# Performance work log

Measured on AMD Instinct MI355X. Metric: run time of the kernel, lower is better.

Reference implementation:

```python
import jax, jax.numpy as jnp
import numpy as np

EPS = 1e-5

def layer_norm(x, g, b):
    m = jnp.mean(x, axis=-1, keepdims=True)
    v = jnp.mean((x - m) ** 2, axis=-1, keepdims=True)
    return (x - m) * jax.lax.rsqrt(v + EPS) * g + b

def setup_inputs() -> dict:
    key = jax.random.key(0)
    ks = jax.random.split(key, 16)
    B, S, IN, D, K = 32, 4096, 256, 64, 8
    inputs = jax.random.normal(ks[0], (B, S, IN), dtype=jnp.float32)
    mask = jnp.ones((B, S), dtype=jnp.int32)
    slot_emb = jax.random.normal(ks[1], (1, K, D), dtype=jnp.float32)
    Wq = jax.random.normal(ks[2], (D, D), dtype=jnp.float32) / np.sqrt(D)
    Wk = jax.random.normal(ks[3], (IN, D), dtype=jnp.float32) / np.sqrt(IN)
    Wv = jax.random.normal(ks[4], (IN, D), dtype=jnp.float32) / np.sqrt(IN)
    W_ih = jax.random.normal(ks[5], (D, 3 * D), dtype=jnp.float32) / np.sqrt(D)
    W_hh = jax.random.normal(ks[6], (D, 3 * D), dtype=jnp.float32) / np.sqrt(D)
    b_ih = jnp.zeros((3 * D,), dtype=jnp.float32)
    b_hh = jnp.zeros((3 * D,), dtype=jnp.float32)
    ln_in_g = jnp.ones((IN,), dtype=jnp.float32)
    ln_in_b = jnp.zeros((IN,), dtype=jnp.float32)
    ln_s_g = jnp.ones((D,), dtype=jnp.float32)
    ln_s_b = jnp.zeros((D,), dtype=jnp.float32)
    Wval = jax.random.normal(ks[7], (D, 1), dtype=jnp.float32) / np.sqrt(D)
    bval = jnp.zeros((1,), dtype=jnp.float32)
    return dict(inputs=inputs, mask=mask, slot_emb=slot_emb, Wq=Wq, Wk=Wk, Wv=Wv,
                W_ih=W_ih, W_hh=W_hh, b_ih=b_ih, b_hh=b_hh,
                ln_in_g=ln_in_g, ln_in_b=ln_in_b, ln_s_g=ln_s_g, ln_s_b=ln_s_b,
                Wval=Wval, bval=bval)

def gru_cell(x, h, W_ih, W_hh, b_ih, b_hh):
    # PyTorch GRUCell: gates ordered (r, z, n)
    gx = x @ W_ih + b_ih
    gh = h @ W_hh + b_hh
    D = h.shape[-1]
    gx_r, gx_z, gx_n = gx[..., :D], gx[..., D:2 * D], gx[..., 2 * D:]
    gh_r, gh_z, gh_n = gh[..., :D], gh[..., D:2 * D], gh[..., 2 * D:]
    r = jax.nn.sigmoid(gx_r + gh_r)
    z = jax.nn.sigmoid(gx_z + gh_z)
    n = jnp.tanh(gx_n + r * gh_n)
    return (1.0 - z) * n + z * h

def reference(inputs, mask, slot_emb, Wq, Wk, Wv, W_ih, W_hh, b_ih, b_hh,
              ln_in_g, ln_in_b, ln_s_g, ln_s_b, Wval, bval):
    B, S, _ = inputs.shape
    K, D = slot_emb.shape[1], slot_emb.shape[2]
    num_iterations = 3
    slots = jnp.broadcast_to(slot_emb, (B, K, D))
    # inputs are constant across iterations: hoist norm + k/v projections
    inputs_norm = layer_norm(inputs, ln_in_g, ln_in_b)
    k = inputs_norm @ Wk  # [B, S, D]
    v = inputs_norm @ Wv  # [B, S, D]
    neg_big = jnp.finfo(inputs.dtype).min
    mask_bks = (mask[:, None, :] == 0)  # [B, 1, S] -> broadcast to [B, K, S]
    scale = 1.0 / np.sqrt(D)
    attn = None
    for _ in range(num_iterations):
        slots_norm = layer_norm(slots, ln_s_g, ln_s_b)
        q = slots_norm @ Wq  # [B, K, D]
        scores = jnp.einsum('bkd,bsd->bks', q, k) * scale
        scores = jnp.where(mask_bks, neg_big, scores)
        attn = jax.nn.softmax(scores, axis=-1)  # [B, K, S]
        updates = jnp.einsum('bks,bsd->bkd', attn, v)  # [B, K, D]
        slots = gru_cell(updates.reshape(-1, D), slots.reshape(-1, D),
                         W_ih, W_hh, b_ih, b_hh).reshape(B, K, D)
    validity = (slots @ Wval + bval)[..., 0]  # [B, K]
    slot_mask = (validity > 0).astype(jnp.float32)  # eval-mode (deterministic) path
    return slots, attn, slot_mask
```

## Files before the change

kernel.cpp:

```cpp
#include <hip/hip_runtime.h>

typedef unsigned short u16;
typedef unsigned int   u32;
typedef _Float16 f16x8 __attribute__((ext_vector_type(8)));
typedef u32    u32x4 __attribute__((ext_vector_type(4)));
typedef float  f32x4 __attribute__((ext_vector_type(4)));

#define NEG_BIG (-3.4028234663852886e38f)
#define LO_SCALE 2048.0f
#define LO_INV   (1.0f/2048.0f)

__device__ __forceinline__ u32 splitpack(float x){
  _Float16 h = (_Float16)x;
  _Float16 l = (_Float16)((x - (float)h) * LO_SCALE);
  return (u32)__builtin_bit_cast(u16, h) | ((u32)__builtin_bit_cast(u16, l) << 16);
}
__device__ __forceinline__ void split2(float x, _Float16& h, _Float16& l){
  h = (_Float16)x;
  l = (_Float16)((x - (float)h) * LO_SCALE);
}
__device__ __forceinline__ void unpack8(const u32* p, f16x8& h, f16x8& l){
  #pragma unroll
  for (int j = 0; j < 8; j++){
    u32 v = p[j];
    h[j] = __builtin_bit_cast(_Float16, (u16)(v & 0xFFFFu));
    l[j] = __builtin_bit_cast(_Float16, (u16)(v >> 16));
  }
}
__device__ __forceinline__ float wsum(float v){
  #pragma unroll
  for (int m = 32; m >= 1; m >>= 1) v += __shfl_xor(v, m, 64);
  return v;
}
__device__ __forceinline__ float wmax(float v){
  #pragma unroll
  for (int m = 32; m >= 1; m >>= 1) v = fmaxf(v, __shfl_xor(v, m, 64));
  return v;
}

__global__ __launch_bounds__(256, 2)
void k_proj(const float* __restrict__ in, const float* __restrict__ g,
            const float* __restrict__ bb, const float* __restrict__ Wk,
            const float* __restrict__ Wv, u32* __restrict__ kws,
            u32* __restrict__ vws)
{
  __shared__ u32 A[64 * 258];
  const int t = threadIdx.x, w = t >> 6, l = t & 63, q = l >> 4, l15 = l & 15;
  const long base = (long)blockIdx.x * 64;

  f32x4 xv[16];
  const f32x4* in4 = (const f32x4*)in;
  #pragma unroll
  for (int i = 0; i < 16; i++) xv[i] = in4[(base + i*4 + w) * 64 + l];

  const f32x4 gv = ((const f32x4*)g)[l];
  const f32x4 bv = ((const f32x4*)bb)[l];

  #pragma unroll
  for (int i = 0; i < 16; i++){
    f32x4 x = xv[i];
    float s  = x.x + x.y + x.z + x.w;
    float ss = x.x*x.x + x.y*x.y + x.z*x.z + x.w*x.w;
    s = wsum(s); ss = wsum(ss);
    float mean = s * (1.f/256.f);
    float var  = fmaxf(ss * (1.f/256.f) - mean*mean, 0.f);
    float rstd = rsqrtf(var + 1e-5f);
    int row = i*4 + w;
    u32x4 o;
    o[0] = splitpack((x.x - mean) * rstd * gv.x + bv.x);
    o[1] = splitpack((x.y - mean) * rstd * gv.y + bv.y);
    o[2] = splitpack((x.z - mean) * rstd * gv.z + bv.z);
    o[3] = splitpack((x.w - mean) * rstd * gv.w + bv.w);
    *(u32x4*)&A[row*258 + l*4] = o;
  }
  __syncthreads();

  f32x4 a1[4][2] = {};
  f32x4 a2[4][2] = {};

  #pragma unroll
  for (int half = 0; half < 2; half++){
    f16x8 bh[2][4], bl[2][4];
    #pragma unroll
    for (int n2 = 0; n2 < 2; n2++){
      const int n = w*32 + n2*16 + l15;
      const float* src = (n < 64) ? (Wk + n) : (Wv + (n - 64));
      #pragma unroll
      for (int k4 = 0; k4 < 4; k4++){
        #pragma unroll
        for (int j = 0; j < 8; j++){
          float wv = src[((half*4 + k4)*32 + q*8 + j) * 64];
          _Float16 h, lo; split2(wv, h, lo);
          bh[n2][k4][j] = h; bl[n2][k4][j] = lo;
        }
      }
    }
    #pragma unroll
    for (int k4 = 0; k4 < 4; k4++){
      const int kt = half*4 + k4;
      f16x8 ah[4], al[4];
      #pragma unroll
      for (int mt = 0; mt < 4; mt++)
        unpack8(&A[(mt*16 + l15)*258 + kt*32 + q*8], ah[mt], al[mt]);
      #pragma unroll
      for (int mt = 0; mt < 4; mt++)
        #pragma unroll
        for (int n2 = 0; n2 < 2; n2++){
          a1[mt][n2] = __builtin_amdgcn_mfma_f32_16x16x32_f16(ah[mt], bh[n2][k4], a1[mt][n2], 0,0,0);
          a2[mt][n2] = __builtin_amdgcn_mfma_f32_16x16x32_f16(ah[mt], bl[n2][k4], a2[mt][n2], 0,0,0);
          a2[mt][n2] = __builtin_amdgcn_mfma_f32_16x16x32_f16(al[mt], bh[n2][k4], a2[mt][n2], 0,0,0);
        }
    }
  }
  __syncthreads();

  #pragma unroll
  for (int mt = 0; mt < 4; mt++)
    #pragma unroll
    for (int n2 = 0; n2 < 2; n2++)
      #pragma unroll
      for (int r = 0; r < 4; r++){
        int row = mt*16 + q*4 + r;
        int col = w*32 + n2*16 + l15;
        A[row*130 + col] = splitpack(a1[mt][n2][r] + a2[mt][n2][r] * LO_INV);
      }
  __syncthreads();

  const int b  = (int)(base >> 12);
  const int s0 = (int)(base & 4095);
  for (int task = t; task < 1024; task += 256){
    int row = task >> 4, seg = task & 15;
    u32x4 val = *(const u32x4*)&A[row*130 + seg*4];
    *(u32x4*)(kws + ((long)b*4096 + s0 + row)*64 + seg*4) = val;
  }
  for (int task = t; task < 1024; task += 256){
    int d = task >> 4, seg = task & 15;
    u32x4 vv;
    #pragma unroll
    for (int j = 0; j < 4; j++) vv[j] = A[(seg*4 + j)*130 + 64 + d];
    *(u32x4*)(vws + ((long)b*64 + d)*4096 + s0 + seg*4) = vv;
  }
}

__global__ __launch_bounds__(256)
void k_attn_part(const float* __restrict__ qws, const u32* __restrict__ kws,
                 const u32* __restrict__ vws, const int* __restrict__ mask,
                 float* __restrict__ scores, float* __restrict__ part)
{
  __shared__ float pl[8 * 256];
  __shared__ u32   pb[16 * 258];
  __shared__ float ml[8];
  const int c = blockIdx.x, b = blockIdx.y;
  const int t = threadIdx.x, w = t >> 6, l = t & 63, q = l >> 4, l15 = l & 15;

  f16x8 qh[2], ql[2];
  #pragma unroll
  for (int kt = 0; kt < 2; kt++){
    #pragma unroll
    for (int j = 0; j < 8; j++){
      int d = kt*32 + q*8 + j;
      float qv = (l15 < 8) ? qws[b*512 + l15*64 + d] : 0.f;
      _Float16 h, lo; split2(qv, h, lo);
      qh[kt][j] = h; ql[kt][j] = lo;
    }
  }
  f32x4 s1[4] = {}, s2[4] = {};
  #pragma unroll
  for (int kt = 0; kt < 2; kt++)
    #pragma unroll
    for (int mt = 0; mt < 4; mt++){
      const u32* kr = kws + ((long)b*4096 + c*256 + w*64 + mt*16 + l15)*64
                      + kt*32 + q*8;
      f16x8 ah, al; unpack8(kr, ah, al);
      s1[mt] = __builtin_amdgcn_mfma_f32_16x16x32_f16(ah, qh[kt], s1[mt], 0,0,0);
      s2[mt] = __builtin_amdgcn_mfma_f32_16x16x32_f16(ah, ql[kt], s2[mt], 0,0,0);
      s2[mt] = __builtin_amdgcn_mfma_f32_16x16x32_f16(al, qh[kt], s2[mt], 0,0,0);
    }
  #pragma unroll
  for (int mt = 0; mt < 4; mt++)
    #pragma unroll
    for (int r = 0; r < 4; r++)
      if (l15 < 8)
        pl[l15*256 + w*64 + mt*16 + q*4 + r] = s1[mt][r] + s2[mt][r] * LO_INV;
  __syncthreads();

  const int s = c*256 + t;
  const int mk = mask[b*4096 + s];
  float sc[8];
  #pragma unroll
  for (int k8 = 0; k8 < 8; k8++){
    float v0 = pl[k8*256 + t] * 0.125f;
    sc[k8] = mk ? v0 : NEG_BIG;
    scores[((long)(b*8 + k8))*4096 + s] = sc[k8];
    pl[k8*256 + t] = sc[k8];
  }
  __syncthreads();

  #pragma unroll
  for (int i = 0; i < 2; i++){
    int slot = w*2 + i;
    float m = fmaxf(fmaxf(pl[slot*256 + l],       pl[slot*256 + 64 + l]),
                    fmaxf(pl[slot*256 + 128 + l], pl[slot*256 + 192 + l]));
    m = wmax(m);
    if (l == 0) ml[slot] = m;
  }
  __syncthreads();

  #pragma unroll
  for (int k8 = 0; k8 < 8; k8++){
    float p = mk ? expf(sc[k8] - ml[k8]) : 0.f;
    pl[k8*256 + t] = p;
    pb[k8*258 + t] = splitpack(p);
  }
  #pragma unroll
  for (int k8 = 8; k8 < 16; k8++) pb[k8*258 + t] = 0;
  __syncthreads();

  #pragma unroll
  for (int i = 0; i < 2; i++){
    int slot = w*2 + i;
    float sm = pl[slot*256 + l] + pl[slot*256 + 64 + l]
             + pl[slot*256 + 128 + l] + pl[slot*256 + 192 + l];
    sm = wsum(sm);
    if (l == 0){
      float* pp = part + ((long)(b*16 + c)*8 + slot)*66;
      pp[0] = ml[slot]; pp[1] = sm;
    }
  }

  f32x4 o1 = {}, o2 = {};
  #pragma unroll
  for (int kt = 0; kt < 8; kt++){
    f16x8 ph, plo; unpack8(&pb[l15*258 + kt*32 + q*8], ph, plo);
    const u32* vr = vws + ((long)b*64 + w*16 + l15)*4096 + c*256 + kt*32 + q*8;
    f16x8 vh, vl; unpack8(vr, vh, vl);
    o1 = __builtin_amdgcn_mfma_f32_16x16x32_f16(ph,  vh, o1, 0,0,0);
    o2 = __builtin_amdgcn_mfma_f32_16x16x32_f16(ph,  vl, o2, 0,0,0);
    o2 = __builtin_amdgcn_mfma_f32_16x16x32_f16(plo, vh, o2, 0,0,0);
  }
  #pragma unroll
  for (int r = 0; r < 4; r++){
    int slot = q*4 + r;
    if (slot < 8)
      part[((long)(b*16 + c)*8 + slot)*66 + 2 + w*16 + l15] = o1[r] + o2[r] * LO_INV;
  }
}

__global__ __launch_bounds__(64)
void k_combine(const float* __restrict__ part, float* __restrict__ slots,
               float* __restrict__ qws, float* __restrict__ mlws,
               const float* __restrict__ W_ih, const float* __restrict__ W_hh,
               const float* __restrict__ b_ih, const float* __restrict__ b_hh,
               const float* __restrict__ g_s, const float* __restrict__ b_s,
               const float* __restrict__ Wq, const float* __restrict__ Wval,
               const float* __restrict__ bval, float* __restrict__ out, int last)
{
  const int row = blockIdx.x;
  const int d = threadIdx.x;
  const int b = row >> 3, kk = row & 7;
  __shared__ float upd_s[64], h_s[64], sn_s[64];

  const float* pp = part + ((long)(b*16)*8 + kk)*66;
  float m = NEG_BIG;
  #pragma unroll
  for (int c = 0; c < 16; c++) m = fmaxf(m, pp[c*528]);
  float lsum = 0.f, o = 0.f;
  #pragma unroll
  for (int c = 0; c < 16; c++){
    const float* pc = pp + c*528;
    float e = expf(pc[0] - m);
    lsum += pc[1] * e;
    o    += pc[2 + d] * e;
  }
  float upd = o / lsum;
  if (last && d == 0){ mlws[row*2] = m; mlws[row*2 + 1] = lsum; }

  float h = slots[row*64 + d];
  upd_s[d] = upd; h_s[d] = h;
  __syncthreads();

  float xr = b_ih[d], xz = b_ih[64 + d], xn = b_ih[128 + d];
  float hr = b_hh[d], hz = b_hh[64 + d], hn = b_hh[128 + d];
  for (int j = 0; j < 64; j++){
    float u = upd_s[j], hh = h_s[j];
    xr += u  * W_ih[j*192 + d];
    xz += u  * W_ih[j*192 + 64 + d];
    xn += u  * W_ih[j*192 + 128 + d];
    hr += hh * W_hh[j*192 + d];
    hz += hh * W_hh[j*192 + 64 + d];
    hn += hh * W_hh[j*192 + 128 + d];
  }
  float r = 1.f / (1.f + expf(-(xr + hr)));
  float z = 1.f / (1.f + expf(-(xz + hz)));
  float n = tanhf(xn + r * hn);
  float hnew = (1.f - z) * n + z * h;
  slots[row*64 + d] = hnew;

  if (!last){
    float s1 = wsum(hnew), s2 = wsum(hnew * hnew);
    float mean = s1 * (1.f/64.f);
    float rstd = rsqrtf(fmaxf(s2 * (1.f/64.f) - mean*mean, 0.f) + 1e-5f);
    float sn = (hnew - mean) * rstd * g_s[d] + b_s[d];
    sn_s[d] = sn;
    __syncthreads();
    float qd = 0.f;
    for (int j = 0; j < 64; j++) qd += sn_s[j] * Wq[j*64 + d];
    qws[row*64 + d] = qd;
  } else {
    out[row*64 + d] = hnew;
    float val = wsum(hnew * Wval[d]);
    if (d == 0)
      out[1064960 + row] = ((val + bval[0]) > 0.f) ? 1.f : 0.f;
  }
}

__global__ __launch_bounds__(64)
void k_init(const float* __restrict__ emb, const float* __restrict__ g_s,
            const float* __restrict__ b_s, const float* __restrict__ Wq,
            float* __restrict__ slots, float* __restrict__ qws)
{
  const int row = blockIdx.x, d = threadIdx.x, kk = row & 7;
  __shared__ float sn_s[64];
  float x = emb[kk*64 + d];
  slots[row*64 + d] = x;
  float s1 = wsum(x), s2 = wsum(x * x);
  float mean = s1 * (1.f/64.f);
  float rstd = rsqrtf(fmaxf(s2 * (1.f/64.f) - mean*mean, 0.f) + 1e-5f);
  float sn = (x - mean) * rstd * g_s[d] + b_s[d];
  sn_s[d] = sn;
  __syncthreads();
  float qd = 0.f;
  for (int j = 0; j < 64; j++) qd += sn_s[j] * Wq[j*64 + d];
  qws[row*64 + d] = qd;
}

__global__ __launch_bounds__(256)
void k_attn_out(const float* __restrict__ scores, const float* __restrict__ mlws,
                float* __restrict__ out)
{
  const int c = blockIdx.x, b = blockIdx.y, t = threadIdx.x;
  const int s = c*256 + t;
  #pragma unroll
  for (int k8 = 0; k8 < 8; k8++){
    int row = b*8 + k8;
    float m = mlws[row*2], lsum = mlws[row*2 + 1];
    float sc = scores[(long)row*4096 + s];
    out[16384 + (long)row*4096 + s] = expf(sc - m) / lsum;
  }
}

extern "C" void kernel_launch(void* const* d_in, const int* in_sizes, int n_in,
                              void* d_out, int out_size, void* d_ws, size_t ws_size,
                              hipStream_t stream)
{
  const float* inputs = (const float*)d_in[0];
  const int*   mask   = (const int*)  d_in[1];
  const float* emb    = (const float*)d_in[2];
  const float* Wq     = (const float*)d_in[3];
  const float* Wk     = (const float*)d_in[4];
  const float* Wv     = (const float*)d_in[5];
  const float* W_ih   = (const float*)d_in[6];
  const float* W_hh   = (const float*)d_in[7];
  const float* b_ih   = (const float*)d_in[8];
  const float* b_hh   = (const float*)d_in[9];
  const float* g_in   = (const float*)d_in[10];
  const float* b_in   = (const float*)d_in[11];
  const float* g_s    = (const float*)d_in[12];
  const float* b_s    = (const float*)d_in[13];
  const float* Wval   = (const float*)d_in[14];
  const float* bval   = (const float*)d_in[15];

  char* ws = (char*)d_ws;
  u32*   kws    = (u32*)  (ws);
  u32*   vws    = (u32*)  (ws + (32ull<<20));
  float* scores = (float*)(ws + (64ull<<20));
  float* part   = (float*)(ws + (68ull<<20));
  float* slots  = (float*)(ws + (70ull<<20));
  float* qws    = (float*)(ws + (70ull<<20) + 65536);
  float* mlws   = (float*)(ws + (70ull<<20) + 131072);

  float* out = (float*)d_out;

  k_proj<<<2048, 256, 0, stream>>>(inputs, g_in, b_in, Wk, Wv, kws, vws);
  k_init<<<256, 64, 0, stream>>>(emb, g_s, b_s, Wq, slots, qws);

  for (int it = 0; it < 3; ++it){
    k_attn_part<<<dim3(16, 32), 256, 0, stream>>>(qws, kws, vws, mask, scores, part);
    k_combine<<<256, 64, 0, stream>>>(part, slots, qws, mlws,
                                      W_ih, W_hh, b_ih, b_hh, g_s, b_s,
                                      Wq, Wval, bval, out, it == 2);
  }
  k_attn_out<<<dim3(16, 32), 256, 0, stream>>>(scores, mlws, out);
}
```

Baseline: 337.0 us.

## Split hi/lo fp16 planes, pre-split weights, shrink proj tile, parallelize combine

K/V are now stored as separate fp16 hi and lo planes instead of interleaved u32 pairs, so the MFMA operands load with vector reads and need no unpacking. A new prep kernel pre-splits Wk/Wv into MFMA-ready fragments, so each projection block no longer does strided weight loads and splits. The projection uses 32-row tiles with higher occupancy, scores are written only on the last iteration, and the GRU combine spreads its reductions over 256 threads. A fourth lo*lo MFMA term is added for accuracy, which adds matrix work in exchange.

```diff
diff --git a/kernel.cpp b/kernel.cpp
--- a/kernel.cpp
+++ b/kernel.cpp
@@ -3,30 +3,21 @@
 typedef unsigned short u16;
 typedef unsigned int   u32;
 typedef _Float16 f16x8 __attribute__((ext_vector_type(8)));
+typedef u16    u16x4 __attribute__((ext_vector_type(4)));
+typedef u16    u16x8 __attribute__((ext_vector_type(8)));
 typedef u32    u32x4 __attribute__((ext_vector_type(4)));
 typedef float  f32x4 __attribute__((ext_vector_type(4)));
 
 #define NEG_BIG (-3.4028234663852886e38f)
 #define LO_SCALE 2048.0f
 #define LO_INV   (1.0f/2048.0f)
-
-__device__ __forceinline__ u32 splitpack(float x){
-  _Float16 h = (_Float16)x;
-  _Float16 l = (_Float16)((x - (float)h) * LO_SCALE);
-  return (u32)__builtin_bit_cast(u16, h) | ((u32)__builtin_bit_cast(u16, l) << 16);
-}
+#define LO_INV2  (1.0f/4194304.0f)
+
 __device__ __forceinline__ void split2(float x, _Float16& h, _Float16& l){
   h = (_Float16)x;
   l = (_Float16)((x - (float)h) * LO_SCALE);
 }
-__device__ __forceinline__ void unpack8(const u32* p, f16x8& h, f16x8& l){
-  #pragma unroll
-  for (int j = 0; j < 8; j++){
-    u32 v = p[j];
-    h[j] = __builtin_bit_cast(_Float16, (u16)(v & 0xFFFFu));
-    l[j] = __builtin_bit_cast(_Float16, (u16)(v >> 16));
-  }
-}
+__device__ __forceinline__ u16 f2u(_Float16 h){ return __builtin_bit_cast(u16, h); }
 __device__ __forceinline__ float wsum(float v){
   #pragma unroll
   for (int m = 32; m >= 1; m >>= 1) v += __shfl_xor(v, m, 64);
@@ -38,26 +29,48 @@
   return v;
 }
 
-__global__ __launch_bounds__(256, 2)
+__global__ __launch_bounds__(256)
+void k_prep(const float* __restrict__ Wk, const float* __restrict__ Wv,
+            u16* __restrict__ Bh, u16* __restrict__ Bl)
+{
+  const int gid = blockIdx.x * 256 + threadIdx.x;
+  const int lane = gid & 63, kt = (gid >> 6) & 7, ntile = gid >> 9;
+  const int q = lane >> 4, l15 = lane & 15;
+  const int n = ntile * 16 + l15;
+  u16x8 hh, ll;
+  #pragma unroll
+  for (int j = 0; j < 8; j++){
+    int k = kt*32 + q*8 + j;
+    float wv = (n < 64) ? Wk[k*64 + n] : Wv[k*64 + (n - 64)];
+    _Float16 h, lo; split2(wv, h, lo);
+    hh[j] = f2u(h); ll[j] = f2u(lo);
+  }
+  *(u16x8*)(Bh + (long)gid*8) = hh;
+  *(u16x8*)(Bl + (long)gid*8) = ll;
+}
+
+__global__ __launch_bounds__(256, 3)
 void k_proj(const float* __restrict__ in, const float* __restrict__ g,
-            const float* __restrict__ bb, const float* __restrict__ Wk,
-            const float* __restrict__ Wv, u32* __restrict__ kws,
-            u32* __restrict__ vws)
-{
-  __shared__ u32 A[64 * 258];
+            const float* __restrict__ bb,
+            const u16* __restrict__ Bh, const u16* __restrict__ Bl,
+            u16* __restrict__ kh, u16* __restrict__ kl,
+            u16* __restrict__ vh, u16* __restrict__ vl)
+{
+  __shared__ __align__(16) u16 Ah[32 * 264];
+  __shared__ __align__(16) u16 Al[32 * 264];
   const int t = threadIdx.x, w = t >> 6, l = t & 63, q = l >> 4, l15 = l & 15;
-  const long base = (long)blockIdx.x * 64;
-
-  f32x4 xv[16];
+  const long base = (long)blockIdx.x * 32;
+
+  f32x4 xv[8];
   const f32x4* in4 = (const f32x4*)in;
   #pragma unroll
-  for (int i = 0; i < 16; i++) xv[i] = in4[(base + i*4 + w) * 64 + l];
+  for (int i = 0; i < 8; i++) xv[i] = in4[(base + i*4 + w) * 64 + l];
 
   const f32x4 gv = ((const f32x4*)g)[l];
   const f32x4 bv = ((const f32x4*)bb)[l];
 
   #pragma unroll
-  for (int i = 0; i < 16; i++){
+  for (int i = 0; i < 8; i++){
     f32x4 x = xv[i];
     float s  = x.x + x.y + x.z + x.w;
     float ss = x.x*x.x + x.y*x.y + x.z*x.z + x.w*x.w;
@@ -66,89 +79,98 @@
     float var  = fmaxf(ss * (1.f/256.f) - mean*mean, 0.f);
     float rstd = rsqrtf(var + 1e-5f);
     int row = i*4 + w;
-    u32x4 o;
-    o[0] = splitpack((x.x - mean) * rstd * gv.x + bv.x);
-    o[1] = splitpack((x.y - mean) * rstd * gv.y + bv.y);
-    o[2] = splitpack((x.z - mean) * rstd * gv.z + bv.z);
-    o[3] = splitpack((x.w - mean) * rstd * gv.w + bv.w);
-    *(u32x4*)&A[row*258 + l*4] = o;
-  }
-  __syncthreads();
-
-  f32x4 a1[4][2] = {};
-  f32x4 a2[4][2] = {};
-
-  #pragma unroll
-  for (int half = 0; half < 2; half++){
-    f16x8 bh[2][4], bl[2][4];
+    float y0 = (x.x - mean) * rstd * gv.x + bv.x;
+    float y1 = (x.y - mean) * rstd * gv.y + bv.y;
+    float y2 = (x.z - mean) * rstd * gv.z + bv.z;
+    float y3 = (x.w - mean) * rstd * gv.w + bv.w;
+    _Float16 h0,l0,h1,l1,h2,l2,h3,l3;
+    split2(y0,h0,l0); split2(y1,h1,l1); split2(y2,h2,l2); split2(y3,h3,l3);
+    u16x4 hv = { f2u(h0), f2u(h1), f2u(h2), f2u(h3) };
+    u16x4 lv = { f2u(l0), f2u(l1), f2u(l2), f2u(l3) };
+    *(u16x4*)&Ah[row*264 + l*4] = hv;
+    *(u16x4*)&Al[row*264 + l*4] = lv;
+  }
+  __syncthreads();
+
+  f32x4 a1[2][2] = {};
+  f32x4 a2[2][2] = {};
+  f32x4 a3[2][2] = {};
+
+  #pragma unroll
+  for (int kt = 0; kt < 8; kt++){
+    f16x8 bhv[2], blv[2];
     #pragma unroll
     for (int n2 = 0; n2 < 2; n2++){
-      const int n = w*32 + n2*16 + l15;
-      const float* src = (n < 64) ? (Wk + n) : (Wv + (n - 64));
+      long idx = ((long)((w*2 + n2)*8 + kt)*64 + l)*8;
+      bhv[n2] = __builtin_bit_cast(f16x8, *(const u32x4*)(Bh + idx));
+      blv[n2] = __builtin_bit_cast(f16x8, *(const u32x4*)(Bl + idx));
+    }
+    f16x8 ahv[2], alv[2];
+    #pragma unroll
+    for (int mt = 0; mt < 2; mt++){
+      int off = (mt*16 + l15)*264 + kt*32 + q*8;
+      ahv[mt] = __builtin_bit_cast(f16x8, *(const u32x4*)&Ah[off]);
+      alv[mt] = __builtin_bit_cast(f16x8, *(const u32x4*)&Al[off]);
+    }
+    #pragma unroll
+    for (int mt = 0; mt < 2; mt++)
       #pragma unroll
-      for (int k4 = 0; k4 < 4; k4++){
-        #pragma unroll
-        for (int j = 0; j < 8; j++){
-          float wv = src[((half*4 + k4)*32 + q*8 + j) * 64];
-          _Float16 h, lo; split2(wv, h, lo);
-          bh[n2][k4][j] = h; bl[n2][k4][j] = lo;
-        }
+      for (int n2 = 0; n2 < 2; n2++){
+        a1[mt][n2] = __builtin_amdgcn_mfma_f32_16x16x32_f16(ahv[mt], bhv[n2], a1[mt][n2], 0,0,0);
+        a2[mt][n2] = __builtin_amdgcn_mfma_f32_16x16x32_f16(ahv[mt], blv[n2], a2[mt][n2], 0,0,0);
+        a2[mt][n2] = __builtin_amdgcn_mfma_f32_16x16x32_f16(alv[mt], bhv[n2], a2[mt][n2], 0,0,0);
+        a3[mt][n2] = __builtin_amdgcn_mfma_f32_16x16x32_f16(alv[mt], blv[n2], a3[mt][n2], 0,0,0);
       }
-    }
-    #pragma unroll
-    for (int k4 = 0; k4 < 4; k4++){
-      const int kt = half*4 + k4;
-      f16x8 ah[4], al[4];
-      #pragma unroll
-      for (int mt = 0; mt < 4; mt++)
-        unpack8(&A[(mt*16 + l15)*258 + kt*32 + q*8], ah[mt], al[mt]);
-      #pragma unroll
-      for (int mt = 0; mt < 4; mt++)
-        #pragma unroll
-        for (int n2 = 0; n2 < 2; n2++){
-          a1[mt][n2] = __builtin_amdgcn_mfma_f32_16x16x32_f16(ah[mt], bh[n2][k4], a1[mt][n2], 0,0,0);
-          a2[mt][n2] = __builtin_amdgcn_mfma_f32_16x16x32_f16(ah[mt], bl[n2][k4], a2[mt][n2], 0,0,0);
-          a2[mt][n2] = __builtin_amdgcn_mfma_f32_16x16x32_f16(al[mt], bh[n2][k4], a2[mt][n2], 0,0,0);
-        }
-    }
-  }
-  __syncthreads();
-
-  #pragma unroll
-  for (int mt = 0; mt < 4; mt++)
+  }
+  __syncthreads();
+
+  #pragma unroll
+  for (int mt = 0; mt < 2; mt++)
     #pragma unroll
     for (int n2 = 0; n2 < 2; n2++)
       #pragma unroll
       for (int r = 0; r < 4; r++){
         int row = mt*16 + q*4 + r;
         int col = w*32 + n2*16 + l15;
-        A[row*130 + col] = splitpack(a1[mt][n2][r] + a2[mt][n2][r] * LO_INV);
+        float val = a1[mt][n2][r] + a2[mt][n2][r]*LO_INV + a3[mt][n2][r]*LO_INV2;
+        _Float16 h, lo; split2(val, h, lo);
+        Ah[row*264 + col] = f2u(h);
+        Al[row*264 + col] = f2u(lo);
       }
   __syncthreads();
 
   const int b  = (int)(base >> 12);
   const int s0 = (int)(base & 4095);
-  for (int task = t; task < 1024; task += 256){
-    int row = task >> 4, seg = task & 15;
-    u32x4 val = *(const u32x4*)&A[row*130 + seg*4];
-    *(u32x4*)(kws + ((long)b*4096 + s0 + row)*64 + seg*4) = val;
-  }
-  for (int task = t; task < 1024; task += 256){
-    int d = task >> 4, seg = task & 15;
-    u32x4 vv;
-    #pragma unroll
-    for (int j = 0; j < 4; j++) vv[j] = A[(seg*4 + j)*130 + 64 + d];
-    *(u32x4*)(vws + ((long)b*64 + d)*4096 + s0 + seg*4) = vv;
+  {
+    int row = t >> 3, seg = t & 7;
+    long o = ((long)b*4096 + s0 + row)*64 + seg*8;
+    *(u16x8*)(kh + o) = *(const u16x8*)&Ah[row*264 + seg*8];
+    *(u16x8*)(kl + o) = *(const u16x8*)&Al[row*264 + seg*8];
+  }
+  {
+    int d = t >> 2, seg = t & 3;
+    u16x8 hv, lv;
+    #pragma unroll
+    for (int j = 0; j < 8; j++){
+      hv[j] = Ah[(seg*8 + j)*264 + 64 + d];
+      lv[j] = Al[(seg*8 + j)*264 + 64 + d];
+    }
+    long o = ((long)b*64 + d)*4096 + s0 + seg*8;
+    *(u16x8*)(vh + o) = hv;
+    *(u16x8*)(vl + o) = lv;
   }
 }
 
 __global__ __launch_bounds__(256)
-void k_attn_part(const float* __restrict__ qws, const u32* __restrict__ kws,
-                 const u32* __restrict__ vws, const int* __restrict__ mask,
-                 float* __restrict__ scores, float* __restrict__ part)
-{
-  __shared__ float pl[8 * 256];
-  __shared__ u32   pb[16 * 258];
+void k_attn_part(const float* __restrict__ qws,
+                 const u16* __restrict__ kh, const u16* __restrict__ kl,
+                 const u16* __restrict__ vh, const u16* __restrict__ vl,
+                 const int* __restrict__ mask,
+                 float* __restrict__ scores, float* __restrict__ part, int last)
+{
+  __shared__ float pl[8 * 257];
+  __shared__ __align__(16) u16 ph[16 * 264];
+  __shared__ __align__(16) u16 plo[16 * 264];
   __shared__ float ml[8];
   const int c = blockIdx.x, b = blockIdx.y;
   const int t = threadIdx.x, w = t >> 6, l = t & 63, q = l >> 4, l15 = l & 15;
@@ -164,24 +186,26 @@
       qh[kt][j] = h; ql[kt][j] = lo;
     }
   }
-  f32x4 s1[4] = {}, s2[4] = {};
+  f32x4 s1[4] = {}, s2[4] = {}, s3[4] = {};
   #pragma unroll
   for (int kt = 0; kt < 2; kt++)
     #pragma unroll
     for (int mt = 0; mt < 4; mt++){
-      const u32* kr = kws + ((long)b*4096 + c*256 + w*64 + mt*16 + l15)*64
-                      + kt*32 + q*8;
-      f16x8 ah, al; unpack8(kr, ah, al);
+      long o = ((long)b*4096 + c*256 + w*64 + mt*16 + l15)*64 + kt*32 + q*8;
+      f16x8 ah = __builtin_bit_cast(f16x8, *(const u32x4*)(kh + o));
+      f16x8 al = __builtin_bit_cast(f16x8, *(const u32x4*)(kl + o));
       s1[mt] = __builtin_amdgcn_mfma_f32_16x16x32_f16(ah, qh[kt], s1[mt], 0,0,0);
       s2[mt] = __builtin_amdgcn_mfma_f32_16x16x32_f16(ah, ql[kt], s2[mt], 0,0,0);
       s2[mt] = __builtin_amdgcn_mfma_f32_16x16x32_f16(al, qh[kt], s2[mt], 0,0,0);
+      s3[mt] = __builtin_amdgcn_mfma_f32_16x16x32_f16(al, ql[kt], s3[mt], 0,0,0);
     }
   #pragma unroll
   for (int mt = 0; mt < 4; mt++)
     #pragma unroll
     for (int r = 0; r < 4; r++)
       if (l15 < 8)
-        pl[l15*256 + w*64 + mt*16 + q*4 + r] = s1[mt][r] + s2[mt][r] * LO_INV;
+        pl[l15*257 + w*64 + mt*16 + q*4 + r] =
+            s1[mt][r] + s2[mt][r]*LO_INV + s3[mt][r]*LO_INV2;
   __syncthreads();
 
   const int s = c*256 + t;
@@ -189,18 +213,18 @@
   float sc[8];
   #pragma unroll
   for (int k8 = 0; k8 < 8; k8++){
-    float v0 = pl[k8*256 + t] * 0.125f;
+    float v0 = pl[k8*257 + t] * 0.125f;
     sc[k8] = mk ? v0 : NEG_BIG;
-    scores[((long)(b*8 + k8))*4096 + s] = sc[k8];
-    pl[k8*256 + t] = sc[k8];
+    if (last) scores[((long)(b*8 + k8))*4096 + s] = sc[k8];
+    pl[k8*257 + t] = sc[k8];
   }
   __syncthreads();
 
   #pragma unroll
   for (int i = 0; i < 2; i++){
     int slot = w*2 + i;
-    float m = fmaxf(fmaxf(pl[slot*256 + l],       pl[slot*256 + 64 + l]),
-                    fmaxf(pl[slot*256 + 128 + l], pl[slot*256 + 192 + l]));
+    float m = fmaxf(fmaxf(pl[slot*257 + l],       pl[slot*257 + 64 + l]),
+                    fmaxf(pl[slot*257 + 128 + l], pl[slot*257 + 192 + l]));
     m = wmax(m);
     if (l == 0) ml[slot] = m;
   }
@@ -209,18 +233,20 @@
   #pragma unroll
   for (int k8 = 0; k8 < 8; k8++){
     float p = mk ? expf(sc[k8] - ml[k8]) : 0.f;
-    pl[k8*256 + t] = p;
-    pb[k8*258 + t] = splitpack(p);
-  }
-  #pragma unroll
-  for (int k8 = 8; k8 < 16; k8++) pb[k8*258 + t] = 0;
+    pl[k8*257 + t] = p;
+    _Float16 h, lo; split2(p, h, lo);
+    ph[k8*264 + t] = f2u(h);
+    plo[k8*264 + t] = f2u(lo);
+  }
+  #pragma unroll
+  for (int k8 = 8; k8 < 16; k8++){ ph[k8*264 + t] = 0; plo[k8*264 + t] = 0; }
   __syncthreads();
 
   #pragma unroll
   for (int i = 0; i < 2; i++){
     int slot = w*2 + i;
-    float sm = pl[slot*256 + l] + pl[slot*256 + 64 + l]
-             + pl[slot*256 + 128 + l] + pl[slot*256 + 192 + l];
+    float sm = pl[slot*257 + l] + pl[slot*257 + 64 + l]
+             + pl[slot*257 + 128 + l] + pl[slot*257 + 192 + l];
     sm = wsum(sm);
     if (l == 0){
       float* pp = part + ((long)(b*16 + c)*8 + slot)*66;
@@ -228,25 +254,30 @@
     }
   }
 
-  f32x4 o1 = {}, o2 = {};
+  f32x4 o1 = {}, o2 = {}, o3 = {};
   #pragma unroll
   for (int kt = 0; kt < 8; kt++){
-    f16x8 ph, plo; unpack8(&pb[l15*258 + kt*32 + q*8], ph, plo);
-    const u32* vr = vws + ((long)b*64 + w*16 + l15)*4096 + c*256 + kt*32 + q*8;
-    f16x8 vh, vl; unpack8(vr, vh, vl);
-    o1 = __builtin_amdgcn_mfma_f32_16x16x32_f16(ph,  vh, o1, 0,0,0);
-    o2 = __builtin_amdgcn_mfma_f32_16x16x32_f16(ph,  vl, o2, 0,0,0);
-    o2 = __builtin_amdgcn_mfma_f32_16x16x32_f16(plo, vh, o2, 0,0,0);
+    int poff = l15*264 + kt*32 + q*8;
+    f16x8 pf = __builtin_bit_cast(f16x8, *(const u32x4*)&ph[poff]);
+    f16x8 pg = __builtin_bit_cast(f16x8, *(const u32x4*)&plo[poff]);
+    long voff = ((long)b*64 + w*16 + l15)*4096 + c*256 + kt*32 + q*8;
+    f16x8 vhf = __builtin_bit_cast(f16x8, *(const u32x4*)(vh + voff));
+    f16x8 vlf = __builtin_bit_cast(f16x8, *(const u32x4*)(vl + voff));
+    o1 = __builtin_amdgcn_mfma_f32_16x16x32_f16(pf, vhf, o1, 0,0,0);
+    o2 = __builtin_amdgcn_mfma_f32_16x16x32_f16(pf, vlf, o2, 0,0,0);
+    o2 = __builtin_amdgcn_mfma_f32_16x16x32_f16(pg, vhf, o2, 0,0,0);
+    o3 = __builtin_amdgcn_mfma_f32_16x16x32_f16(pg, vlf, o3, 0,0,0);
   }
   #pragma unroll
   for (int r = 0; r < 4; r++){
     int slot = q*4 + r;
     if (slot < 8)
-      part[((long)(b*16 + c)*8 + slot)*66 + 2 + w*16 + l15] = o1[r] + o2[r] * LO_INV;
-  }
-}
-
-__global__ __launch_bounds__(64)
+      part[((long)(b*16 + c)*8 + slot)*66 + 2 + w*16 + l15] =
+          o1[r] + o2[r]*LO_INV + o3[r]*LO_INV2;
+  }
+}
+
+__global__ __launch_bounds__(256)
 void k_combine(const float* __restrict__ part, float* __restrict__ slots,
                float* __restrict__ qws, float* __restrict__ mlws,
                const float* __restrict__ W_ih, const float* __restrict__ W_hh,
@@ -256,9 +287,12 @@
                const float* __restrict__ bval, float* __restrict__ out, int last)
 {
   const int row = blockIdx.x;
-  const int d = threadIdx.x;
+  const int t = threadIdx.x;
+  const int d = t & 63, jg = t >> 6;
   const int b = row >> 3, kk = row & 7;
-  __shared__ float upd_s[64], h_s[64], sn_s[64];
+  __shared__ float redO[4][64], redL[4][64];
+  __shared__ float redG[4][6][64];
+  __shared__ float upd_s[64], h_s[64], hn_s[64], sn_s[64];
 
   const float* pp = part + ((long)(b*16)*8 + kk)*66;
   float m = NEG_BIG;
@@ -266,51 +300,82 @@
   for (int c = 0; c < 16; c++) m = fmaxf(m, pp[c*528]);
   float lsum = 0.f, o = 0.f;
   #pragma unroll
-  for (int c = 0; c < 16; c++){
-    const float* pc = pp + c*528;
+  for (int ci = 0; ci < 4; ci++){
+    const float* pc = pp + (jg*4 + ci)*528;
     float e = expf(pc[0] - m);
     lsum += pc[1] * e;
     o    += pc[2 + d] * e;
   }
-  float upd = o / lsum;
-  if (last && d == 0){ mlws[row*2] = m; mlws[row*2 + 1] = lsum; }
-
-  float h = slots[row*64 + d];
-  upd_s[d] = upd; h_s[d] = h;
-  __syncthreads();
-
-  float xr = b_ih[d], xz = b_ih[64 + d], xn = b_ih[128 + d];
-  float hr = b_hh[d], hz = b_hh[64 + d], hn = b_hh[128 + d];
-  for (int j = 0; j < 64; j++){
+  redO[jg][d] = o; redL[jg][d] = lsum;
+  __syncthreads();
+  if (jg == 0){
+    float oo = redO[0][d] + redO[1][d] + redO[2][d] + redO[3][d];
+    float ll = redL[0][d] + redL[1][d] + redL[2][d] + redL[3][d];
+    upd_s[d] = oo / ll;
+    h_s[d] = slots[row*64 + d];
+    if (last && d == 0){ mlws[row*2] = m; mlws[row*2 + 1] = ll; }
+  }
+  __syncthreads();
+
+  float a0=0,a1=0,a2=0,a3=0,a4=0,a5=0;
+  #pragma unroll
+  for (int ji = 0; ji < 16; ji++){
+    int j = jg*16 + ji;
     float u = upd_s[j], hh = h_s[j];
-    xr += u  * W_ih[j*192 + d];
-    xz += u  * W_ih[j*192 + 64 + d];
-    xn += u  * W_ih[j*192 + 128 + d];
-    hr += hh * W_hh[j*192 + d];
-    hz += hh * W_hh[j*192 + 64 + d];
-    hn += hh * W_hh[j*192 + 128 + d];
-  }
-  float r = 1.f / (1.f + expf(-(xr + hr)));
-  float z = 1.f / (1.f + expf(-(xz + hz)));
-  float n = tanhf(xn + r * hn);
-  float hnew = (1.f - z) * n + z * h;
-  slots[row*64 + d] = hnew;
+    a0 += u  * W_ih[j*192 + d];
+    a1 += u  * W_ih[j*192 + 64 + d];
+    a2 += u  * W_ih[j*192 + 128 + d];
+    a3 += hh * W_hh[j*192 + d];
+    a4 += hh * W_hh[j*192 + 64 + d];
+    a5 += hh * W_hh[j*192 + 128 + d];
+  }
+  redG[jg][0][d]=a0; redG[jg][1][d]=a1; redG[jg][2][d]=a2;
+  redG[jg][3][d]=a3; redG[jg][4][d]=a4; redG[jg][5][d]=a5;
+  __syncthreads();
+
+  if (jg == 0){
+    float xr = b_ih[d]       + redG[0][0][d]+redG[1][0][d]+redG[2][0][d]+redG[3][0][d];
+    float xz = b_ih[64 + d]  + redG[0][1][d]+redG[1][1][d]+redG[2][1][d]+redG[3][1][d];
+    float xn = b_ih[128 + d] + redG[0][2][d]+redG[1][2][d]+redG[2][2][d]+redG[3][2][d];
+    float hr = b_hh[d]       + redG[0][3][d]+redG[1][3][d]+redG[2][3][d]+redG[3][3][d];
+    float hz = b_hh[64 + d]  + redG[0][4][d]+redG[1][4][d]+redG[2][4][d]+redG[3][4][d];
+    float hn = b_hh[128 + d] + redG[0][5][d]+redG[1][5][d]+redG[2][5][d]+redG[3][5][d];
+    float r = 1.f / (1.f + expf(-(xr + hr)));
+    float z = 1.f / (1.f + expf(-(xz + hz)));
+    float n = tanhf(xn + r * hn);
+    float h = h_s[d];
+    float hnew = (1.f - z) * n + z * h;
+    slots[row*64 + d] = hnew;
+    hn_s[d] = hnew;
+  }
+  __syncthreads();
 
   if (!last){
-    float s1 = wsum(hnew), s2 = wsum(hnew * hnew);
+    float hv = hn_s[d];
+    float s1 = wsum(hv), s2 = wsum(hv * hv);
     float mean = s1 * (1.f/64.f);
     float rstd = rsqrtf(fmaxf(s2 * (1.f/64.f) - mean*mean, 0.f) + 1e-5f);
-    float sn = (hnew - mean) * rstd * g_s[d] + b_s[d];
-    sn_s[d] = sn;
+    float sn = (hv - mean) * rstd * g_s[d] + b_s[d];
+    if (jg == 0) sn_s[d] = sn;
     __syncthreads();
     float qd = 0.f;
-    for (int j = 0; j < 64; j++) qd += sn_s[j] * Wq[j*64 + d];
-    qws[row*64 + d] = qd;
+    #pragma unroll
+    for (int ji = 0; ji < 16; ji++){
+      int j = jg*16 + ji;
+      qd += sn_s[j] * Wq[j*64 + d];
+    }
+    redO[jg][d] = qd;
+    __syncthreads();
+    if (jg == 0)
+      qws[row*64 + d] = redO[0][d] + redO[1][d] + redO[2][d] + redO[3][d];
   } else {
-    out[row*64 + d] = hnew;
-    float val = wsum(hnew * Wval[d]);
-    if (d == 0)
-      out[1064960 + row] = ((val + bval[0]) > 0.f) ? 1.f : 0.f;
+    if (jg == 0){
+      float hv = hn_s[d];
+      out[row*64 + d] = hv;
+      float val = wsum(hv * Wval[d]);
+      if (d == 0)
+        out[1064960 + row] = ((val + bval[0]) > 0.f) ? 1.f : 0.f;
+    }
   }
 }
 
@@ -371,24 +436,31 @@
   const float* bval   = (const float*)d_in[15];
 
   char* ws = (char*)d_ws;
-  u32*   kws    = (u32*)  (ws);
-  u32*   vws    = (u32*)  (ws + (32ull<<20));
-  float* scores = (float*)(ws + (64ull<<20));
-  float* part   = (float*)(ws + (68ull<<20));
-  float* slots  = (float*)(ws + (70ull<<20));
-  float* qws    = (float*)(ws + (70ull<<20) + 65536);
-  float* mlws   = (float*)(ws + (70ull<<20) + 131072);
+  const unsigned long MiB = 1ull << 20;
+  u16*   kh     = (u16*)  (ws);
+  u16*   kl     = (u16*)  (ws + 16*MiB);
+  u16*   vh     = (u16*)  (ws + 32*MiB);
+  u16*   vl     = (u16*)  (ws + 48*MiB);
+  u16*   Bh     = (u16*)  (ws + 64*MiB);
+  u16*   Bl     = (u16*)  (ws + 64*MiB + 65536);
+  float* scores = (float*)(ws + 64*MiB + 131072);
+  float* part   = (float*)(ws + 68*MiB + 131072);
+  float* slots  = (float*)(ws + 69*MiB + 131072 + 0x110000);
+  float* qws    = (float*)(ws + 69*MiB + 131072 + 0x110000 + 65536);
+  float* mlws   = (float*)(ws + 69*MiB + 131072 + 0x110000 + 131072);
 
   float* out = (float*)d_out;
 
-  k_proj<<<2048, 256, 0, stream>>>(inputs, g_in, b_in, Wk, Wv, kws, vws);
+  k_prep<<<16, 256, 0, stream>>>(Wk, Wv, Bh, Bl);
+  k_proj<<<4096, 256, 0, stream>>>(inputs, g_in, b_in, Bh, Bl, kh, kl, vh, vl);
   k_init<<<256, 64, 0, stream>>>(emb, g_s, b_s, Wq, slots, qws);
 
   for (int it = 0; it < 3; ++it){
-    k_attn_part<<<dim3(16, 32), 256, 0, stream>>>(qws, kws, vws, mask, scores, part);
-    k_combine<<<256, 64, 0, stream>>>(part, slots, qws, mlws,
-                                      W_ih, W_hh, b_ih, b_hh, g_s, b_s,
-                                      Wq, Wval, bval, out, it == 2);
+    k_attn_part<<<dim3(16, 32), 256, 0, stream>>>(qws, kh, kl, vh, vl, mask,
+                                                  scores, part, it == 2);
+    k_combine<<<256, 256, 0, stream>>>(part, slots, qws, mlws,
+                                       W_ih, W_hh, b_ih, b_hh, g_s, b_s,
+                                       Wq, Wval, bval, out, it == 2);
   }
   k_attn_out<<<dim3(16, 32), 256, 0, stream>>>(scores, mlws, out);
 }
```

Measured after the change: 322.2 us. 4.4% less time.
